# Kernel optimization log

Measured on AMD Instinct MI355X. Metric: run time of the kernel, lower is better.

## Reference

```python
import jax, jax.numpy as jnp
import numpy as np

B, S, D, H = 32, 577, 768, 12
DH = D // H
MLP = 4 * D
EPS = 1e-5


def _layernorm(x, g, b):
    m = jnp.mean(x, axis=-1, keepdims=True)
    v = jnp.mean((x - m) ** 2, axis=-1, keepdims=True)
    return (x - m) * jax.lax.rsqrt(v + EPS) * g + b


def setup_inputs() -> dict:
    key = jax.random.key(0)
    ks = jax.random.split(key, 12)
    w = lambda k, shp: (jax.random.normal(k, shp, dtype=jnp.float32) * 0.02)
    return {
        "x": jax.random.normal(ks[0], (B, S, D), dtype=jnp.float32),
        "ln1_g": jnp.ones((D,), jnp.float32), "ln1_b": jnp.zeros((D,), jnp.float32),
        "ln2_g": jnp.ones((D,), jnp.float32), "ln2_b": jnp.zeros((D,), jnp.float32),
        "wq": w(ks[1], (H, DH, DH)), "bq": jnp.zeros((H, DH), jnp.float32),
        "wk": w(ks[2], (H, DH, DH)), "bk": jnp.zeros((H, DH), jnp.float32),
        "wv": w(ks[3], (H, DH, DH)), "bv": jnp.zeros((H, DH), jnp.float32),
        "w1": w(ks[4], (D, MLP)), "b1": jnp.zeros((MLP,), jnp.float32),
        "w2": w(ks[5], (MLP, D)), "b2": jnp.zeros((D,), jnp.float32),
    }


def reference(x, ln1_g, ln1_b, ln2_g, ln2_b, wq, bq, wk, bk, wv, bv, w1, b1, w2, b2):
    b, s, d = x.shape
    xn = _layernorm(x, ln1_g, ln1_b)
    xh = xn.reshape(b, s, H, DH)  # split heads along last dim (as in torch slicing)
    # per-head linear maps, batched over heads: [B,H,S,DH]
    q = jnp.einsum('bshd,hdo->bhso', xh, wq) + bq[:, None, :]
    k = jnp.einsum('bshd,hdo->bhso', xh, wk) + bk[:, None, :]
    v = jnp.einsum('bshd,hdo->bhso', xh, wv) + bv[:, None, :]
    scores = jnp.einsum('bhso,bhto->bhst', q, k) / (DH ** 0.5)
    attn = jax.nn.softmax(scores, axis=-1)  # softmax over keys (torch dim=1 of [S,S])
    o = jnp.einsum('bhst,bhtd->bshd', attn, v).reshape(b, s, d)
    out = x + o
    yn = _layernorm(out, ln2_g, ln2_b)
    h = jax.nn.gelu(yn @ w1 + b1, approximate=False)  # torch GELU default is erf-based
    return out + h @ w2 + b2
```

## Files before the change

### kernel.cpp

```cpp
#include <hip/hip_runtime.h>

#define S_LEN 577
#define SPAD  640
#define DMODEL 768
#define NH 12
#define DHEAD 64
#define MLPD 3072
#define NROWS (32 * 577)
#define MPAD  18688
#define NBH   (32 * 12)
#define LOG2E 1.44269504088896340736f

typedef __attribute__((ext_vector_type(8))) short s8v;
typedef __attribute__((ext_vector_type(4))) float f4v;

#define MFMA16(a, b, c) __builtin_amdgcn_mfma_f32_16x16x32_bf16((a), (b), (c), 0, 0, 0)

__device__ __forceinline__ short f2bf(float f) {
  union { float f; unsigned u; } a; a.f = f;
  unsigned r = a.u + 0x7FFFu + ((a.u >> 16) & 1u);
  return (short)(r >> 16);
}
__device__ __forceinline__ short f2bfF(float f) {
  union { float f; unsigned u; } a; a.f = f;
  return (short)((a.u + 0x8000u) >> 16);
}

__device__ __forceinline__ void gload16(const short* g, const short* l) {
  __builtin_amdgcn_global_load_lds(
      (const __attribute__((address_space(1))) void*)g,
      (__attribute__((address_space(3))) void*)l, 16, 0, 0);
}

__global__ __launch_bounds__(256) void transpose_w(const float* __restrict__ in,
                                                   short* __restrict__ out, int R, int C) {
  __shared__ float tile[32][33];
  int c0 = blockIdx.x * 32, r0 = blockIdx.y * 32;
  int tx = threadIdx.x, ty = threadIdx.y;
  for (int i = ty; i < 32; i += 8) tile[i][tx] = in[(size_t)(r0 + i) * C + c0 + tx];
  __syncthreads();
  for (int i = ty; i < 32; i += 8) out[(size_t)(c0 + i) * R + r0 + tx] = f2bf(tile[tx][i]);
}

__global__ __launch_bounds__(256) void prep_qkv(const float* __restrict__ wq, const float* __restrict__ wk,
                                                const float* __restrict__ wv, short* __restrict__ oq,
                                                short* __restrict__ ok, short* __restrict__ ov) {
  int h = blockIdx.x, t = threadIdx.x;
  const float* src0 = wq + (size_t)h * 4096;
  const float* src1 = wk + (size_t)h * 4096;
  const float* src2 = wv + (size_t)h * 4096;
  short* dst0 = oq + (size_t)h * 4096;
  short* dst1 = ok + (size_t)h * 4096;
  short* dst2 = ov + (size_t)h * 4096;
  for (int i = t; i < 4096; i += 256) {
    int o = i >> 6, d = i & 63;
    dst0[i] = f2bf(src0[d * 64 + o]);
    dst1[i] = f2bf(src1[d * 64 + o]);
    dst2[i] = f2bf(src2[d * 64 + o]);
  }
}

__global__ __launch_bounds__(256) void pad_kv(short* __restrict__ kg, short* __restrict__ vt) {
  int idx = blockIdx.x * 256 + threadIdx.x;
  const int padw = SPAD - S_LEN;
  const int per = DHEAD * padw;
  if (idx >= NBH * per) return;
  int bh = idx / per, r = idx - bh * per;
  int col = r / padw, s = S_LEN + (r - col * padw);
  vt[((size_t)bh * DHEAD + col) * SPAD + s] = 0;
  kg[((size_t)bh * SPAD + s) * DHEAD + col] = 0;
}

__global__ __launch_bounds__(256) void ln_kernel(const float* __restrict__ x, const float* __restrict__ g,
                                                 const float* __restrict__ bta, short* __restrict__ out) {
  int row = blockIdx.x;
  int t = threadIdx.x;
  const float* xr = x + (size_t)row * DMODEL;
  float v0 = xr[t], v1 = xr[t + 256], v2 = xr[t + 512];
  float s = v0 + v1 + v2;
  float s2 = v0 * v0 + v1 * v1 + v2 * v2;
  for (int o = 32; o; o >>= 1) { s += __shfl_down(s, o); s2 += __shfl_down(s2, o); }
  __shared__ float red[8];
  if ((t & 63) == 0) { int w = t >> 6; red[w] = s; red[4 + w] = s2; }
  __syncthreads();
  s = red[0] + red[1] + red[2] + red[3];
  s2 = red[4] + red[5] + red[6] + red[7];
  float m = s * (1.f / DMODEL);
  float rs = rsqrtf(s2 * (1.f / DMODEL) - m * m + 1e-5f);
  short* orow = out + (size_t)row * DMODEL;
  orow[t]       = f2bf((v0 - m) * rs * g[t]       + bta[t]);
  orow[t + 256] = f2bf((v1 - m) * rs * g[t + 256] + bta[t + 256]);
  orow[t + 512] = f2bf((v2 - m) * rs * g[t + 512] + bta[t + 512]);
}

__global__ __launch_bounds__(256) void qkv_kernel(const short* __restrict__ xn,
    const short* __restrict__ wqt, const short* __restrict__ wkt, const short* __restrict__ wvt,
    const float* __restrict__ bq, const float* __restrict__ bk, const float* __restrict__ bv,
    short* __restrict__ qg, short* __restrict__ kg, short* __restrict__ vt) {
  __shared__ __align__(16) short wl[3][64][72];
  int bid = blockIdx.x;
  int h = bid % NH, mt = bid / NH;
  int t = threadIdx.x;
  {
    int o = t >> 2, d0 = (t & 3) * 16;
    const short* s0 = wqt + (size_t)h * 4096 + o * 64 + d0;
    const short* s1 = wkt + (size_t)h * 4096 + o * 64 + d0;
    const short* s2 = wvt + (size_t)h * 4096 + o * 64 + d0;
    *(uint4*)&wl[0][o][d0]     = *(const uint4*)s0;
    *(uint4*)&wl[0][o][d0 + 8] = *(const uint4*)(s0 + 8);
    *(uint4*)&wl[1][o][d0]     = *(const uint4*)s1;
    *(uint4*)&wl[1][o][d0 + 8] = *(const uint4*)(s1 + 8);
    *(uint4*)&wl[2][o][d0]     = *(const uint4*)s2;
    *(uint4*)&wl[2][o][d0 + 8] = *(const uint4*)(s2 + 8);
  }
  __syncthreads();
  int w = t >> 6, l = t & 63, l15 = l & 15, lh = l >> 4;
  int m0 = mt * 64 + w * 16;
  if (m0 >= NROWS) return;
  f4v z = {0.f, 0.f, 0.f, 0.f};
  f4v aq[4], ak[4], av[4];
#pragma unroll
  for (int nt = 0; nt < 4; ++nt) { aq[nt] = z; ak[nt] = z; av[nt] = z; }
  const short* xrow = xn + (size_t)(m0 + l15) * DMODEL + h * DHEAD;
#pragma unroll
  for (int kk = 0; kk < 64; kk += 32) {
    s8v af = *(const s8v*)(xrow + kk + lh * 8);
#pragma unroll
    for (int nt = 0; nt < 4; ++nt) {
      s8v b0 = *(const s8v*)&wl[0][nt * 16 + l15][kk + lh * 8];
      s8v b1 = *(const s8v*)&wl[1][nt * 16 + l15][kk + lh * 8];
      s8v b2 = *(const s8v*)&wl[2][nt * 16 + l15][kk + lh * 8];
      aq[nt] = MFMA16(af, b0, aq[nt]);
      ak[nt] = MFMA16(af, b1, ak[nt]);
      av[nt] = MFMA16(af, b2, av[nt]);
    }
  }
#pragma unroll
  for (int nt = 0; nt < 4; ++nt) {
    int col = nt * 16 + l15;
    float biq = bq[h * DHEAD + col], bik = bk[h * DHEAD + col], biv = bv[h * DHEAD + col];
#pragma unroll
    for (int i = 0; i < 4; ++i) {
      int m = m0 + lh * 4 + i;
      int bb = m / S_LEN;
      int ss = m - bb * S_LEN;
      int bh = bb * NH + h;
      qg[((size_t)bh * S_LEN + ss) * DHEAD + col] = f2bf((aq[nt][i] + biq) * (0.125f * LOG2E));
      kg[((size_t)bh * SPAD + ss) * DHEAD + col]  = f2bf(ak[nt][i] + bik);
      vt[((size_t)bh * DHEAD + col) * SPAD + ss]  = f2bf(av[nt][i] + biv);
    }
  }
}

__global__ __launch_bounds__(256) void attn_kernel(const short* __restrict__ qg, const short* __restrict__ kg,
                                                   const short* __restrict__ vt, const float* __restrict__ x,
                                                   float* __restrict__ outp) {
  __shared__ __align__(16) short Pb[4][32][72];
  int bh = blockIdx.x;
  int qt = blockIdx.y;
  int h = bh % NH, b = bh / NH;
  int t = threadIdx.x, w = t >> 6, l = t & 63, l15 = l & 15, lh = l >> 4;
  int q0 = qt * 128 + w * 32;
  if (q0 > 576) return;
  size_t qbase = (size_t)bh * S_LEN * DHEAD;
  size_t kbase = (size_t)bh * SPAD * DHEAD;
  size_t vbase = (size_t)bh * DHEAD * SPAD;
  s8v aq[2][2];
#pragma unroll
  for (int f = 0; f < 2; ++f) {
    int qrow = q0 + f * 16 + l15; if (qrow > 576) qrow = 576;
    const short* qp = qg + qbase + (size_t)qrow * DHEAD + lh * 8;
    aq[f][0] = *(const s8v*)qp;
    aq[f][1] = *(const s8v*)(qp + 32);
  }
  f4v z = {0.f, 0.f, 0.f, 0.f};
  f4v z16 = {-16.f, -16.f, -16.f, -16.f};
  f4v acc[2][4];
  float lsum[2][4];
#pragma unroll
  for (int f = 0; f < 2; ++f) {
#pragma unroll
    for (int dt = 0; dt < 4; ++dt) acc[f][dt] = z;
#pragma unroll
    for (int i = 0; i < 4; ++i) lsum[f][i] = 0.f;
  }

#define LOADK(KB, K0, K1)                                              \
  {                                                                    \
    _Pragma("unroll")                                                  \
    for (int nt = 0; nt < 4; ++nt) {                                   \
      const short* kp = kg + kbase + (size_t)((KB) + nt * 16 + l15) * DHEAD + lh * 8; \
      K0[nt] = *(const s8v*)kp;                                        \
      K1[nt] = *(const s8v*)(kp + 32);                                 \
    }                                                                  \
  }

  s8v kf0[4], kf1[4];
  LOADK(0, kf0, kf1);

  for (int kt = 0; kt < 10; ++kt) {
    int kb = kt * 64;
    f4v sc[2][4];
#pragma unroll
    for (int nt = 0; nt < 4; ++nt) {
#pragma unroll
      for (int f = 0; f < 2; ++f) {
        f4v a = MFMA16(aq[f][0], kf0[nt], z16);
        a = MFMA16(aq[f][1], kf1[nt], a);
        sc[f][nt] = a;
      }
    }
    s8v kn0[4], kn1[4];
    if (kt < 9) LOADK(kb + 64, kn0, kn1);
    if (kt == 9) {
#pragma unroll
      for (int nt = 0; nt < 4; ++nt) {
        int col = kb + nt * 16 + l15;
        if (col > 576) {
#pragma unroll
          for (int f = 0; f < 2; ++f) { sc[f][nt][0] = sc[f][nt][1] = sc[f][nt][2] = sc[f][nt][3] = -1e30f; }
        }
      }
    }
#pragma unroll
    for (int f = 0; f < 2; ++f)
#pragma unroll
      for (int i = 0; i < 4; ++i) {
        float s = lsum[f][i];
#pragma unroll
        for (int nt = 0; nt < 4; ++nt) {
          float e = exp2f(sc[f][nt][i]);
          s += e;
          Pb[w][f * 16 + lh * 4 + i][nt * 16 + l15] = f2bfF(e);
        }
        lsum[f][i] = s;
      }
#pragma unroll
    for (int kk2 = 0; kk2 < 2; ++kk2) {
      const short* vp = vt + vbase + kb + kk2 * 32 + lh * 8;
      s8v af0 = *(const s8v*)&Pb[w][l15][kk2 * 32 + lh * 8];
      s8v af1 = *(const s8v*)&Pb[w][16 + l15][kk2 * 32 + lh * 8];
#pragma unroll
      for (int dt = 0; dt < 4; ++dt) {
        s8v bf = *(const s8v*)(vp + (size_t)(dt * 16 + l15) * SPAD);
        acc[0][dt] = MFMA16(af0, bf, acc[0][dt]);
        acc[1][dt] = MFMA16(af1, bf, acc[1][dt]);
      }
    }
#pragma unroll
    for (int nt = 0; nt < 4; ++nt) { kf0[nt] = kn0[nt]; kf1[nt] = kn1[nt]; }
  }
#undef LOADK
#pragma unroll
  for (int f = 0; f < 2; ++f)
#pragma unroll
    for (int i = 0; i < 4; ++i) {
      float s = lsum[f][i];
      s += __shfl_xor(s, 1);
      s += __shfl_xor(s, 2);
      s += __shfl_xor(s, 4);
      s += __shfl_xor(s, 8);
      int srow = q0 + f * 16 + lh * 4 + i;
      if (srow > 576) continue;
      float inv = 1.f / s;
      size_t idx0 = ((size_t)b * S_LEN + srow) * DMODEL + h * DHEAD + l15;
#pragma unroll
      for (int dt = 0; dt < 4; ++dt) {
        size_t idx = idx0 + dt * 16;
        outp[idx] = x[idx] + acc[f][dt][i] * inv;
      }
    }
}

#define BARR asm volatile("s_barrier" ::: "memory")

#define STAGE_HALF(G, SH, bufi, half, ktile)                                       \
  do {                                                                             \
    _Pragma("unroll") for (int rd = 0; rd < 2; ++rd) {                             \
      int rw_ = rd * 64 + (tid >> 3);                                              \
      int sl_ = (tid & 7) ^ (rw_ & 7);                                             \
      gload16((G) + (size_t)((half) * 128 + rw_) * K + (ktile) * 64 + sl_ * 8,     \
              &SH[bufi][(half) * 128 + rw_][(tid & 7) * 8]);                       \
    }                                                                              \
  } while (0)

#define READ_A(rh)                                                                 \
  _Pragma("unroll") for (int mt = 0; mt < 4; ++mt)                                 \
    _Pragma("unroll") for (int kh = 0; kh < 2; ++kh)                               \
      af[mt][kh] = *(const s8v*)&sA[cur][(rh) * 128 + wr * 64 + mt * 16 + l15]     \
                                    [((kh * 4 + lh) ^ s7) * 8];

#define READ_B(BF, chh)                                                            \
  _Pragma("unroll") for (int nt = 0; nt < 2; ++nt)                                 \
    _Pragma("unroll") for (int kh = 0; kh < 2; ++kh)                               \
      BF[nt][kh] = *(const s8v*)&sB[cur][wc * 64 + (chh) * 32 + nt * 16 + l15]     \
                                    [((kh * 4 + lh) ^ s7) * 8];

#define DO_MFMA(rh, ch, BF)                                                        \
  __builtin_amdgcn_s_setprio(1);                                                   \
  _Pragma("unroll") for (int mt = 0; mt < 4; ++mt)                                 \
    _Pragma("unroll") for (int nt = 0; nt < 2; ++nt)                               \
      _Pragma("unroll") for (int kh = 0; kh < 2; ++kh)                             \
        acc[(rh) * 4 + mt][(ch) * 2 + nt] =                                        \
            MFMA16(af[mt][kh], BF[nt][kh], acc[(rh) * 4 + mt][(ch) * 2 + nt]);     \
  __builtin_amdgcn_s_setprio(0);

#define GEMM8_BODY                                                                 \
  int nwg = gridDim.x;                                                             \
  int orig = blockIdx.x;                                                           \
  int qq = nwg >> 3, rr = nwg & 7;                                                 \
  int xcd = orig & 7, lin = orig >> 3;                                             \
  int wg = (xcd < rr ? xcd * (qq + 1) : rr * (qq + 1) + (xcd - rr) * qq) + lin;    \
  int nx = N >> 8;                                                                 \
  int n0 = (wg % nx) * 256, m0 = (wg / nx) * 256;                                  \
  int tid = threadIdx.x;                                                           \
  int wid = tid >> 6, l = tid & 63, l15 = l & 15, lh = l >> 4;                     \
  int s7 = l15 & 7;                                                                \
  int wr = wid >> 2, wc = wid & 3;                                                 \
  const short* Ab = A + (size_t)m0 * K;                                            \
  const short* Bb = Bt + (size_t)n0 * K;                                           \
  f4v z = {0.f, 0.f, 0.f, 0.f};                                                    \
  f4v acc[8][4];                                                                   \
  _Pragma("unroll") for (int i = 0; i < 8; ++i)                                    \
    _Pragma("unroll") for (int j = 0; j < 4; ++j) acc[i][j] = z;                   \
  s8v af[4][2], bf0[2][2], bf1[2][2];                                              \
  int NT = K >> 6;                                                                 \
  STAGE_HALF(Ab, sA, 0, 0, 0); STAGE_HALF(Ab, sA, 0, 1, 0);                        \
  STAGE_HALF(Bb, sB, 0, 0, 0); STAGE_HALF(Bb, sB, 0, 1, 0);                        \
  STAGE_HALF(Ab, sA, 1, 0, 1); STAGE_HALF(Bb, sB, 1, 0, 1);                        \
  STAGE_HALF(Bb, sB, 1, 1, 1);                                                     \
  asm volatile("s_waitcnt vmcnt(6)" ::: "memory");                                 \
  BARR;                                                                            \
  int cur = 0;                                                                     \
  for (int kt = 0; kt < NT; ++kt) {                                                \
    int nxt = cur ^ 1;                                                             \
    READ_A(0); READ_B(bf0, 0);                                                     \
    if (kt + 1 < NT) STAGE_HALF(Ab, sA, nxt, 1, kt + 1);                           \
    BARR; DO_MFMA(0, 0, bf0); BARR;                                                \
    READ_B(bf1, 1);                                                                \
    if (kt + 2 < NT) STAGE_HALF(Ab, sA, cur, 0, kt + 2);                           \
    BARR; DO_MFMA(0, 1, bf1); BARR;                                                \
    READ_A(1);                                                                     \
    if (kt + 2 < NT) STAGE_HALF(Bb, sB, cur, 0, kt + 2);                           \
    BARR; DO_MFMA(1, 1, bf1); BARR;                                                \
    if (kt + 2 < NT) STAGE_HALF(Bb, sB, cur, 1, kt + 2);                           \
    BARR; DO_MFMA(1, 0, bf0);                                                      \
    if (kt < NT - 2)       { asm volatile("s_waitcnt vmcnt(6)" ::: "memory"); }    \
    else if (kt == NT - 2) { asm volatile("s_waitcnt vmcnt(0)" ::: "memory"); }    \
    BARR;                                                                          \
    cur = nxt;                                                                     \
  }

__global__ __launch_bounds__(512, 1) void gemm_gelu(const short* __restrict__ A, const short* __restrict__ Bt,
                                                    const float* __restrict__ bias, short* __restrict__ C,
                                                    int M, int N, int K) {
  __shared__ __align__(16) short sA[2][256][64];
  __shared__ __align__(16) short sB[2][256][64];
  GEMM8_BODY
#pragma unroll
  for (int ri = 0; ri < 8; ++ri)
#pragma unroll
    for (int ci = 0; ci < 4; ++ci) {
      int col = n0 + wc * 64 + (ci >> 1) * 32 + (ci & 1) * 16 + l15;
      float bi = bias[col];
#pragma unroll
      for (int i = 0; i < 4; ++i) {
        int row = m0 + (ri >> 2) * 128 + wr * 64 + (ri & 3) * 16 + lh * 4 + i;
        float v = acc[ri][ci][i] + bi;
        float u = v * (2.30221838f + 0.10294364f * v * v);
        v = v / (1.f + exp2f(-u));
        C[(size_t)row * N + col] = f2bf(v);
      }
    }
}

__global__ __launch_bounds__(512, 1) void gemm_res(const short* __restrict__ A, const short* __restrict__ Bt,
                                                   const float* __restrict__ bias, float* __restrict__ outp,
                                                   int Mvalid, int N, int K) {
  __shared__ __align__(16) short sA[2][256][64];
  __shared__ __align__(16) short sB[2][256][64];
  GEMM8_BODY
#pragma unroll
  for (int ri = 0; ri < 8; ++ri)
#pragma unroll
    for (int ci = 0; ci < 4; ++ci) {
      int col = n0 + wc * 64 + (ci >> 1) * 32 + (ci & 1) * 16 + l15;
      float bi = bias[col];
#pragma unroll
      for (int i = 0; i < 4; ++i) {
        int row = m0 + (ri >> 2) * 128 + wr * 64 + (ri & 3) * 16 + lh * 4 + i;
        if (row < Mvalid) {
          size_t idx = (size_t)row * N + col;
          outp[idx] += acc[ri][ci][i] + bi;
        }
      }
    }
}

extern "C" void kernel_launch(void* const* d_in, const int* in_sizes, int n_in,
                              void* d_out, int out_size, void* d_ws, size_t ws_size,
                              hipStream_t stream) {
  const float* x    = (const float*)d_in[0];
  const float* ln1g = (const float*)d_in[1];
  const float* ln1b = (const float*)d_in[2];
  const float* ln2g = (const float*)d_in[3];
  const float* ln2b = (const float*)d_in[4];
  const float* wq   = (const float*)d_in[5];
  const float* bq   = (const float*)d_in[6];
  const float* wk   = (const float*)d_in[7];
  const float* bk   = (const float*)d_in[8];
  const float* wv   = (const float*)d_in[9];
  const float* bv   = (const float*)d_in[10];
  const float* w1   = (const float*)d_in[11];
  const float* b1   = (const float*)d_in[12];
  const float* w2   = (const float*)d_in[13];
  const float* b2   = (const float*)d_in[14];
  float* outp = (float*)d_out;

  char* ws = (char*)d_ws;
  size_t off = 0;
  auto carve = [&](size_t elems) -> short* {
    short* p = (short*)(ws + off);
    off += elems * sizeof(short);
    off = (off + 255) & ~(size_t)255;
    return p;
  };
  short* yn   = carve((size_t)MPAD * DMODEL);
  short* w1t  = carve((size_t)MLPD * DMODEL);
  short* w2t  = carve((size_t)DMODEL * MLPD);
  short* wqt  = carve((size_t)NH * 64 * 64);
  short* wkt  = carve((size_t)NH * 64 * 64);
  short* wvt  = carve((size_t)NH * 64 * 64);
  size_t union_base = off;
  short* hbuf = carve((size_t)MPAD * MLPD);
  off = union_base;
  short* xn   = carve((size_t)NROWS * DMODEL);
  short* qg   = carve((size_t)NBH * S_LEN * DHEAD);
  short* kg   = carve((size_t)NBH * SPAD * DHEAD);
  short* vtb  = carve((size_t)NBH * DHEAD * SPAD);
  (void)ws_size; (void)in_sizes; (void)n_in; (void)out_size;

  transpose_w<<<dim3(MLPD / 32, DMODEL / 32), dim3(32, 8), 0, stream>>>(w1, w1t, DMODEL, MLPD);
  transpose_w<<<dim3(DMODEL / 32, MLPD / 32), dim3(32, 8), 0, stream>>>(w2, w2t, MLPD, DMODEL);
  prep_qkv<<<NH, 256, 0, stream>>>(wq, wk, wv, wqt, wkt, wvt);
  pad_kv<<<(NBH * DHEAD * (SPAD - S_LEN) + 255) / 256, 256, 0, stream>>>(kg, vtb);

  ln_kernel<<<NROWS, 256, 0, stream>>>(x, ln1g, ln1b, xn);

  qkv_kernel<<<((NROWS + 63) / 64) * NH, 256, 0, stream>>>(xn, wqt, wkt, wvt, bq, bk, bv, qg, kg, vtb);

  attn_kernel<<<dim3(NBH, 5), 256, 0, stream>>>(qg, kg, vtb, x, outp);

  ln_kernel<<<NROWS, 256, 0, stream>>>(outp, ln2g, ln2b, yn);

  gemm_gelu<<<dim3((MPAD / 256) * (MLPD / 256)), 512, 0, stream>>>(yn, w1t, b1, hbuf, MPAD, MLPD, DMODEL);
  gemm_res<<<dim3((MPAD / 256) * (DMODEL / 256)), 512, 0, stream>>>(hbuf, w2t, b2, outp, NROWS, DMODEL, MLPD);
}
```

Measured before the change: 528.3 us.

## Software-pipeline attention loop: compute next QK tile and softmax before current PV

Restructures the attention key loop so that the QK^T MFMAs and exp/softmax for tile kt+1 run before the PV MFMAs of tile kt. P is double-buffered in LDS, and V fragments are loaded into registers early. The aim is to overlap the exp and LDS-write latency with MFMA work and to hide V load latency. The cost is higher register pressure (extra V and K fragments) and twice the LDS for P.

```diff
diff --git a/kernel.cpp b/kernel.cpp
--- a/kernel.cpp
+++ b/kernel.cpp
@@ -155,7 +155,7 @@
 __global__ __launch_bounds__(256) void attn_kernel(const short* __restrict__ qg, const short* __restrict__ kg,
                                                    const short* __restrict__ vt, const float* __restrict__ x,
                                                    float* __restrict__ outp) {
-  __shared__ __align__(16) short Pb[4][32][72];
+  __shared__ __align__(16) short Pb[4][2][32][72];
   int bh = blockIdx.x;
   int qt = blockIdx.y;
   int h = bh % NH, b = bh / NH;
@@ -195,62 +195,86 @@
     }                                                                  \
   }
 
-  s8v kf0[4], kf1[4];
+#define QKTILE(MASK)                                                   \
+  {                                                                    \
+    _Pragma("unroll")                                                  \
+    for (int nt = 0; nt < 4; ++nt) {                                   \
+      _Pragma("unroll")                                                \
+      for (int f = 0; f < 2; ++f) {                                    \
+        f4v a = MFMA16(aq[f][0], kf0[nt], z16);                        \
+        a = MFMA16(aq[f][1], kf1[nt], a);                              \
+        sc[f][nt] = a;                                                 \
+      }                                                                \
+    }                                                                  \
+    if (MASK) {                                                        \
+      _Pragma("unroll")                                                \
+      for (int nt = 0; nt < 4; ++nt) {                                 \
+        int col = 576 + nt * 16 + l15;                                 \
+        if (col > 576) {                                               \
+          _Pragma("unroll")                                            \
+          for (int f = 0; f < 2; ++f) {                                \
+            sc[f][nt][0] = sc[f][nt][1] = sc[f][nt][2] = sc[f][nt][3] = -1e30f; } \
+        }                                                              \
+      }                                                                \
+    }                                                                  \
+  }
+
+#define SMAX(PAR)                                                      \
+  {                                                                    \
+    _Pragma("unroll")                                                  \
+    for (int f = 0; f < 2; ++f)                                        \
+      _Pragma("unroll")                                                \
+      for (int i = 0; i < 4; ++i) {                                    \
+        float s = lsum[f][i];                                          \
+        _Pragma("unroll")                                              \
+        for (int nt = 0; nt < 4; ++nt) {                               \
+          float e = exp2f(sc[f][nt][i]);                               \
+          s += e;                                                      \
+          Pb[w][PAR][f * 16 + lh * 4 + i][nt * 16 + l15] = f2bfF(e);   \
+        }                                                              \
+        lsum[f][i] = s;                                                \
+      }                                                                \
+  }
+
+  s8v kf0[4], kf1[4], kn0[4], kn1[4];
+  f4v sc[2][4];
   LOADK(0, kf0, kf1);
+  QKTILE(false);
+  LOADK(64, kn0, kn1);
+  SMAX(0);
 
   for (int kt = 0; kt < 10; ++kt) {
+    int par = kt & 1;
     int kb = kt * 64;
-    f4v sc[2][4];
-#pragma unroll
-    for (int nt = 0; nt < 4; ++nt) {
-#pragma unroll
-      for (int f = 0; f < 2; ++f) {
-        f4v a = MFMA16(aq[f][0], kf0[nt], z16);
-        a = MFMA16(aq[f][1], kf1[nt], a);
-        sc[f][nt] = a;
-      }
-    }
-    s8v kn0[4], kn1[4];
-    if (kt < 9) LOADK(kb + 64, kn0, kn1);
-    if (kt == 9) {
-#pragma unroll
-      for (int nt = 0; nt < 4; ++nt) {
-        int col = kb + nt * 16 + l15;
-        if (col > 576) {
-#pragma unroll
-          for (int f = 0; f < 2; ++f) { sc[f][nt][0] = sc[f][nt][1] = sc[f][nt][2] = sc[f][nt][3] = -1e30f; }
-        }
-      }
-    }
-#pragma unroll
-    for (int f = 0; f < 2; ++f)
-#pragma unroll
-      for (int i = 0; i < 4; ++i) {
-        float s = lsum[f][i];
-#pragma unroll
-        for (int nt = 0; nt < 4; ++nt) {
-          float e = exp2f(sc[f][nt][i]);
-          s += e;
-          Pb[w][f * 16 + lh * 4 + i][nt * 16 + l15] = f2bfF(e);
-        }
-        lsum[f][i] = s;
-      }
+    s8v vf[2][4];
 #pragma unroll
     for (int kk2 = 0; kk2 < 2; ++kk2) {
       const short* vp = vt + vbase + kb + kk2 * 32 + lh * 8;
-      s8v af0 = *(const s8v*)&Pb[w][l15][kk2 * 32 + lh * 8];
-      s8v af1 = *(const s8v*)&Pb[w][16 + l15][kk2 * 32 + lh * 8];
+#pragma unroll
+      for (int dt = 0; dt < 4; ++dt)
+        vf[kk2][dt] = *(const s8v*)(vp + (size_t)(dt * 16 + l15) * SPAD);
+    }
+    if (kt < 9) {
+#pragma unroll
+      for (int nt = 0; nt < 4; ++nt) { kf0[nt] = kn0[nt]; kf1[nt] = kn1[nt]; }
+      QKTILE(kt + 1 == 9);
+      if (kt < 8) LOADK(kb + 128, kn0, kn1);
+      SMAX(par ^ 1);
+    }
+#pragma unroll
+    for (int kk2 = 0; kk2 < 2; ++kk2) {
+      s8v af0 = *(const s8v*)&Pb[w][par][l15][kk2 * 32 + lh * 8];
+      s8v af1 = *(const s8v*)&Pb[w][par][16 + l15][kk2 * 32 + lh * 8];
 #pragma unroll
       for (int dt = 0; dt < 4; ++dt) {
-        s8v bf = *(const s8v*)(vp + (size_t)(dt * 16 + l15) * SPAD);
-        acc[0][dt] = MFMA16(af0, bf, acc[0][dt]);
-        acc[1][dt] = MFMA16(af1, bf, acc[1][dt]);
+        acc[0][dt] = MFMA16(af0, vf[kk2][dt], acc[0][dt]);
+        acc[1][dt] = MFMA16(af1, vf[kk2][dt], acc[1][dt]);
       }
     }
-#pragma unroll
-    for (int nt = 0; nt < 4; ++nt) { kf0[nt] = kn0[nt]; kf1[nt] = kn1[nt]; }
   }
 #undef LOADK
+#undef QKTILE
+#undef SMAX
 #pragma unroll
   for (int f = 0; f < 2; ++f)
 #pragma unroll
```

Result: no change. 533.4 us (+1.0%).
